# Kernel tuning notes

Measured on AMD Instinct MI355X. Metric: run time of the kernel, lower is better.

The kernel has to match this reference:

```python
import jax, jax.numpy as jnp
import numpy as np

N, E, C, ED = 50000, 800000, 128, 16
NEG_SLOPE = 0.2


def setup_inputs() -> dict:
    key = jax.random.key(0)
    ks = jax.random.split(key, 18)
    inp = {
        "h": jax.random.normal(ks[0], (N, C), jnp.float32),
        "edge_index": jax.random.randint(ks[1], (2, E), 0, N),
        "edge_attr": jax.random.normal(ks[2], (E, ED), jnp.float32),
        "reducible": jax.random.randint(ks[3], (N,), 0, 2) > 0,
    }
    names = ["W", "att_src", "att_dst", "W_edge", "att_edge", "W_res", "bias"]
    shapes = [(C, C), (C,), (C,), (ED, C), (C,), (C, C), (C,)]
    i = 4
    for pre in ["red_", "irr_"]:
        for n, sh in zip(names, shapes):
            inp[pre + n] = jax.random.normal(ks[i], sh, jnp.float32) * 0.05
            i += 1
    return inp


def _gat_conv(h, src, dst, edge_attr, W, att_src, att_dst, W_edge, att_edge, W_res, bias):
    """PyG GATConv (heads=1, residual=True, add_self_loops=True, fill_value='mean')."""
    n = h.shape[0]
    # self-loop edge_attr = mean of incoming edge_attr per node (0 if none)
    sum_attr = jax.ops.segment_sum(edge_attr, dst, num_segments=n)
    cnt = jax.ops.segment_sum(jnp.ones((edge_attr.shape[0],), edge_attr.dtype), dst, num_segments=n)
    mean_attr = sum_attr / jnp.maximum(cnt, 1.0)[:, None]
    loop = jnp.arange(n)
    s = jnp.concatenate([src, loop])   # [E+N]
    d = jnp.concatenate([dst, loop])   # [E+N]
    ea = jnp.concatenate([edge_attr, mean_attr], axis=0)  # [E+N, ED]
    x = h @ W                              # [N, C]
    a_src = x @ att_src                    # [N]
    a_dst = x @ att_dst                    # [N]
    a_edge = (ea @ W_edge) @ att_edge      # [E+N]
    alpha = jax.nn.leaky_relu(a_src[s] + a_dst[d] + a_edge, NEG_SLOPE)
    # per-destination softmax (every node has a self-loop -> denom > 0)
    m = jax.ops.segment_max(alpha, d, num_segments=n)
    ex = jnp.exp(alpha - m[d])
    denom = jax.ops.segment_sum(ex, d, num_segments=n)
    w = ex / denom[d]                      # [E+N]
    out = jax.ops.segment_sum(w[:, None] * x[s], d, num_segments=n)  # [N, C]
    return out + h @ W_res + bias


def reference(h, edge_index, edge_attr, reducible,
              red_W, red_att_src, red_att_dst, red_W_edge, red_att_edge, red_W_res, red_bias,
              irr_W, irr_att_src, irr_att_dst, irr_W_edge, irr_att_edge, irr_W_res, irr_bias):
    src, dst = edge_index[0], edge_index[1]
    out_r = _gat_conv(h, src, dst, edge_attr, red_W, red_att_src, red_att_dst,
                      red_W_edge, red_att_edge, red_W_res, red_bias)
    out_i = _gat_conv(h, src, dst, edge_attr, irr_W, irr_att_src, irr_att_dst,
                      irr_W_edge, irr_att_edge, irr_W_res, irr_bias)
    return jax.nn.relu(jnp.where(reducible[:, None], out_r, out_i))
```

## Files before the change

### kernel.cpp

```cpp
#include <hip/hip_runtime.h>
#include <hip/hip_bf16.h>

#define CDIM 128
#define EDIM 16
#define NEG_SLOPE 0.2f

typedef __attribute__((ext_vector_type(8))) short bf16x8;
typedef __attribute__((ext_vector_type(4))) float f32x4;
typedef unsigned int uint;
typedef unsigned short ushort;

__device__ __forceinline__ ushort f2bf(float f) {
    uint u = __float_as_uint(f);
    return (ushort)((u + 0x7fffu + ((u >> 16) & 1u)) >> 16);
}
__device__ __forceinline__ uint packbf(float lo, float hi) {
    return ((uint)f2bf(hi) << 16) | (uint)f2bf(lo);
}
__device__ __forceinline__ float bflo(uint w) { return __uint_as_float(w << 16); }
__device__ __forceinline__ float bfhi(uint w) { return __uint_as_float(w & 0xffff0000u); }

__device__ __forceinline__ bool redtest(const void* red, int i, int notInt, int notFloat) {
    if (!notInt)        return ((const int*)red)[i] != 0;
    else if (!notFloat) return ((const float*)red)[i] != 0.f;
    else                return ((const unsigned char*)red)[i] != 0;
}

__global__ void bcatwe_kernel(const float* __restrict__ Wr, const float* __restrict__ Wi,
                              const float* __restrict__ Wrr, const float* __restrict__ Wri,
                              ushort* __restrict__ BT,
                              const float* __restrict__ WeR, const float* __restrict__ aeR,
                              const float* __restrict__ WeI, const float* __restrict__ aeI,
                              float* __restrict__ we) {
    if (blockIdx.x < 256) {
        int idx = blockIdx.x * 256 + threadIdx.x;
        int c = idx >> 7, k = idx & 127;
        const float* srcm;
        if (c < 128)      srcm = Wr;
        else if (c < 256) srcm = Wi;
        else if (c < 384) srcm = Wrr;
        else              srcm = Wri;
        BT[idx] = f2bf(srcm[k * 128 + (c & 127)]);
    } else {
        int lane = threadIdx.x;
        if (lane < 16) {
            float s = 0.f;
            for (int c = 0; c < CDIM; ++c) s += WeR[lane * CDIM + c] * aeR[c];
            we[lane] = s;
        } else if (lane < 32) {
            int j = lane - 16;
            float s = 0.f;
            for (int c = 0; c < CDIM; ++c) s += WeI[j * CDIM + c] * aeI[c];
            we[16 + j] = s;
        }
    }
}

__global__ __launch_bounds__(256) void prep_kernel(const uint* __restrict__ red, int nwords,
                                                   int* __restrict__ flags,
                                                   const int* __restrict__ dst, int* __restrict__ cnt,
                                                   int* __restrict__ rank,
                                                   const float* __restrict__ ea, const float* __restrict__ we,
                                                   uint* __restrict__ escal4, int E) {
    int i = blockIdx.x * 256 + threadIdx.x;
    if (i < nwords) {
        uint w = red[i];
        bool isInt = (w <= 1u);
        bool isFloat = (w == 0u) || (w == 0x3f800000u);
        if (!isInt) atomicOr(&flags[0], 1);
        if (!isFloat) atomicOr(&flags[1], 1);
    }
    if (i < E) {
        rank[i] = atomicAdd(&cnt[dst[i]], 1);
        const float4* row = (const float4*)(ea + (size_t)i * EDIM);
        const float4* we4 = (const float4*)we;
        float er = 0.f, ei = 0.f;
#pragma unroll
        for (int q = 0; q < 4; ++q) {
            float4 v = row[q];
            float4 wr = we4[q], wi = we4[4 + q];
            er += v.x * wr.x + v.y * wr.y + v.z * wr.z + v.w * wr.w;
            ei += v.x * wi.x + v.y * wi.y + v.z * wi.z + v.w * wi.w;
        }
        escal4[i] = packbf(er, ei);
    }
}

__global__ __launch_bounds__(512) void gemm_fused(const float* __restrict__ h,
                                                  const ushort* __restrict__ BT,
                                                  ushort* __restrict__ C,
                                                  const float* __restrict__ attsr, const float* __restrict__ attdr,
                                                  const float* __restrict__ attsi, const float* __restrict__ attdi,
                                                  float* __restrict__ asr, float* __restrict__ adr,
                                                  float* __restrict__ asi, float* __restrict__ adi, int M) {
    __shared__ ushort Bs[512 * 128];
    __shared__ ushort As[64 * 128];
    __shared__ float dots[4][64];
    int t = threadIdx.x, lane = t & 63, wv = t >> 6;
    int rb = blockIdx.x * 64;
    int l15 = lane & 15, l4 = lane >> 4;

    if (t < 256) dots[t >> 6][t & 63] = 0.f;

#pragma unroll
    for (int p = 0; p < 16; ++p) {
        int g = wv * 16 + p;
        int col = g * 4 + l4;
        int chs = l15 ^ (col & 7);
        const ushort* gb = BT + col * 128 + chs * 8;
        __builtin_amdgcn_global_load_lds(
            (const __attribute__((address_space(1))) void*)gb,
            (__attribute__((address_space(3))) void*)((char*)Bs + g * 1024), 16, 0, 0);
    }

    {
        int row = t >> 3, cp = (t & 7) * 2;
        int gr = rb + row; if (gr > M - 1) gr = M - 1;
        const float4* hp = (const float4*)(h + (size_t)gr * 128 + cp * 8);
        float4 v0 = hp[0], v1 = hp[1], v2 = hp[2], v3 = hp[3];
        uint4 u0, u1;
        u0.x = packbf(v0.x, v0.y); u0.y = packbf(v0.z, v0.w);
        u0.z = packbf(v1.x, v1.y); u0.w = packbf(v1.z, v1.w);
        u1.x = packbf(v2.x, v2.y); u1.y = packbf(v2.z, v2.w);
        u1.z = packbf(v3.x, v3.y); u1.w = packbf(v3.z, v3.w);
        *(uint4*)((char*)As + row * 256 + ((cp)     ^ (row & 7)) * 16) = u0;
        *(uint4*)((char*)As + row * 256 + ((cp + 1) ^ (row & 7)) * 16) = u1;
    }
    __syncthreads();

    f32x4 acc[4][4];
#pragma unroll
    for (int i = 0; i < 4; ++i)
#pragma unroll
        for (int j = 0; j < 4; ++j) acc[i][j] = (f32x4){0.f, 0.f, 0.f, 0.f};

    const char* Ab = (const char*)As;
    const char* Bb = (const char*)Bs;
#pragma unroll
    for (int ks = 0; ks < 4; ++ks) {
        bf16x8 a[4], b[4];
#pragma unroll
        for (int f = 0; f < 4; ++f) {
            int row = f * 16 + l15;
            int ch = (ks * 4 + l4) ^ (row & 7);
            a[f] = *(const bf16x8*)(Ab + row * 256 + ch * 16);
            int col = wv * 64 + f * 16 + l15;
            int ch2 = (ks * 4 + l4) ^ (col & 7);
            b[f] = *(const bf16x8*)(Bb + col * 256 + ch2 * 16);
        }
#pragma unroll
        for (int i = 0; i < 4; ++i)
#pragma unroll
            for (int j = 0; j < 4; ++j)
                acc[i][j] = __builtin_amdgcn_mfma_f32_16x16x32_bf16(a[i], b[j], acc[i][j], 0, 0, 0);
    }

    if (wv < 4) {
        int var = wv >> 1;
        const float* attS = var ? attsi : attsr;
        const float* attD = var ? attdi : attdr;
        float aS[4], aD[4];
#pragma unroll
        for (int j = 0; j < 4; ++j) {
            int c = (wv & 1) * 64 + j * 16 + l15;
            aS[j] = attS[c]; aD[j] = attD[c];
        }
#pragma unroll
        for (int i = 0; i < 4; ++i)
#pragma unroll
            for (int rr = 0; rr < 4; ++rr) {
                float ps = 0.f, pd = 0.f;
#pragma unroll
                for (int j = 0; j < 4; ++j) {
                    float v = acc[i][j][rr];
                    ps += v * aS[j]; pd += v * aD[j];
                }
#pragma unroll
                for (int d = 1; d < 16; d <<= 1) {
                    ps += __shfl_xor(ps, d); pd += __shfl_xor(pd, d);
                }
                if (l15 == 0) {
                    int row = i * 16 + l4 * 4 + rr;
                    atomicAdd(&dots[var * 2 + 0][row], ps);
                    atomicAdd(&dots[var * 2 + 1][row], pd);
                }
            }
    }

#pragma unroll
    for (int i = 0; i < 4; ++i) {
#pragma unroll
        for (int j = 0; j < 4; ++j) {
            int col = wv * 64 + j * 16 + l15;
#pragma unroll
            for (int r = 0; r < 4; ++r) {
                int gr = rb + i * 16 + l4 * 4 + r;
                if (gr < M) C[(size_t)gr * 512 + col] = f2bf(acc[i][j][r]);
            }
        }
    }

    __syncthreads();
    if (t < 256) {
        int arr = t >> 6, row = t & 63;
        int gr = rb + row;
        if (gr < M) {
            float v = dots[arr][row];
            if (arr == 0)      asr[gr] = v;
            else if (arr == 1) adr[gr] = v;
            else if (arr == 2) asi[gr] = v;
            else               adi[gr] = v;
        }
    }
}

__global__ __launch_bounds__(256) void scanA_kernel(const int* __restrict__ cnt,
                                                    int* __restrict__ offv,
                                                    int* __restrict__ bsum, int n) {
    __shared__ int wsum[4];
    int t = threadIdx.x, lane = t & 63, wid = t >> 6;
    int i0 = blockIdx.x * 1024 + t * 4;
    int v[4];
#pragma unroll
    for (int j = 0; j < 4; ++j) { int i = i0 + j; v[j] = (i < n) ? cnt[i] : 0; }
    int s = v[0] + v[1] + v[2] + v[3];
    int incl = s;
#pragma unroll
    for (int d = 1; d < 64; d <<= 1) { int u = __shfl_up(incl, d); if (lane >= d) incl += u; }
    if (lane == 63) wsum[wid] = incl;
    __syncthreads();
    int wpre = 0;
    for (int w = 0; w < wid; ++w) wpre += wsum[w];
    int run = wpre + incl - s;
#pragma unroll
    for (int j = 0; j < 4; ++j) {
        int i = i0 + j;
        if (i < n) offv[i] = run;
        run += v[j];
    }
    if (t == 255) bsum[blockIdx.x] = wpre + incl;
}

__global__ void scanB_kernel(int* __restrict__ bsum, int* __restrict__ offv, int nb, int n) {
    int lane = threadIdx.x;
    int carry = 0;
    for (int base = 0; base < nb; base += 64) {
        int i = base + lane;
        int v = (i < nb) ? bsum[i] : 0;
        int incl = v;
#pragma unroll
        for (int d = 1; d < 64; d <<= 1) { int u = __shfl_up(incl, d); if (lane >= d) incl += u; }
        if (i < nb) bsum[i] = carry + incl - v;
        carry += __shfl(incl, 63);
    }
    if (lane == 0) offv[n] = carry;
}

__global__ __launch_bounds__(256) void scanC_kernel(int* __restrict__ offv,
                                                    const int* __restrict__ bsum, int n) {
    int add = bsum[blockIdx.x];
    int i0 = blockIdx.x * 1024 + threadIdx.x * 4;
#pragma unroll
    for (int j = 0; j < 4; ++j) {
        int i = i0 + j;
        if (i < n) offv[i] += add;
    }
}

__global__ __launch_bounds__(256) void scatter_kernel(
    const int* __restrict__ src, const int* __restrict__ dst,
    const int* __restrict__ rank, const uint* __restrict__ escal4,
    const void* __restrict__ red, const int* __restrict__ flags,
    const int* __restrict__ offv, uint* __restrict__ csr, int E) {
    int e = blockIdx.x * 256 + threadIdx.x;
    if (e >= E) return;
    int s = src[e], d = dst[e];
    uint ee = escal4[e];
    int notInt = flags[0], notFloat = flags[1];
    bool rr = redtest(red, d, notInt, notFloat);
    uint evb = rr ? (ee & 0xffffu) : (ee >> 16);
    csr[offv[d] + rank[e]] = (uint)s | (evb << 16);
}

__global__ __launch_bounds__(256) void node_kernel(
    const ushort* __restrict__ xcat,
    const float* __restrict__ adst_r, const float* __restrict__ adst_i,
    const float* __restrict__ asrc_r, const float* __restrict__ asrc_i,
    const void* __restrict__ red, const int* __restrict__ flags,
    const int* __restrict__ offv, const uint* __restrict__ csr,
    const float* __restrict__ bias_r, const float* __restrict__ bias_i,
    float* __restrict__ out, int n) {
    __shared__ uint2 buf[4][64];
    int wv = threadIdx.x >> 6, lane = threadIdx.x & 63;
    int node = blockIdx.x * 4 + wv;
    if (node >= n) return;

    int notInt = flags[0], notFloat = flags[1];
    bool r = redtest(red, node, notInt, notFloat);

    const float* asrc = r ? asrc_r : asrc_i;
    float adst = (r ? adst_r : adst_i)[node];
    uint vsel = r ? 0u : 256u;
    int b0 = offv[node], b1 = offv[node + 1];
    int k = b1 - b0;
    const char* xb = (const char*)xcat;
    uint lane4 = lane * 4;

    float m = -1e30f, denom = 0.f;
    float acc0a = 0.f, acc1a = 0.f, acc0b = 0.f, acc1b = 0.f;
    float sumE = 0.f;

    for (int base = b0; base < b1; base += 64) {
        int j = base + lane;
        float al = -1e30f; uint soff = 0;
        if (j < b1) {
            uint rec = csr[j];
            uint s = rec & 0xffffu;
            float ev = bfhi(rec);
            sumE += ev;
            soff = s * 1024u + vsel;
            float a = asrc[s] + ev + adst;
            al = (a >= 0.f) ? a : NEG_SLOPE * a;
        }
        float cm = al;
#pragma unroll
        for (int d = 32; d; d >>= 1) cm = fmaxf(cm, __shfl_xor(cm, d));
        float mn = fmaxf(m, cm);
        float sc = __expf(m - mn);
        denom *= sc; acc0a *= sc; acc1a *= sc; acc0b *= sc; acc1b *= sc;
        m = mn;
        float ex = (j < b1) ? __expf(al - mn) : 0.f;
        buf[wv][lane] = make_uint2(__float_as_uint(ex), soff);
        __builtin_amdgcn_wave_barrier();
        int cc = min(64, b1 - base);
        int ccp = (cc + 7) & ~7;
        for (int tq = 0; tq < ccp; tq += 8) {
            uint2 u[8];
#pragma unroll
            for (int q = 0; q < 8; ++q) u[q] = buf[wv][tq + q];
            uint v[8];
#pragma unroll
            for (int q = 0; q < 8; ++q) v[q] = *(const uint*)(xb + u[q].y + lane4);
#pragma unroll
            for (int q = 0; q < 4; ++q) {
                float w = __uint_as_float(u[q].x);
                acc0a += w * bflo(v[q]); acc1a += w * bfhi(v[q]);
            }
#pragma unroll
            for (int q = 4; q < 8; ++q) {
                float w = __uint_as_float(u[q].x);
                acc0b += w * bflo(v[q]); acc1b += w * bfhi(v[q]);
            }
        }
        float exs = ex;
#pragma unroll
        for (int d = 32; d; d >>= 1) exs += __shfl_xor(exs, d);
        denom += exs;
        __builtin_amdgcn_wave_barrier();
    }
    float acc0 = acc0a + acc0b, acc1 = acc1a + acc1b;

#pragma unroll
    for (int d = 32; d; d >>= 1) sumE += __shfl_xor(sumE, d);
    float eself = sumE / fmaxf((float)k, 1.f);
    float a = asrc[node] + adst + eself;
    float aself = (a >= 0.f) ? a : NEG_SLOPE * a;
    float mn = fmaxf(m, aself);
    float sc = __expf(m - mn);
    float exl = __expf(aself - mn);
    denom = denom * sc + exl;
    uint voff = (uint)node * 1024u + vsel;
    uint vsw = *(const uint*)(xb + voff + lane4);
    acc0 = acc0 * sc + exl * bflo(vsw);
    acc1 = acc1 * sc + exl * bfhi(vsw);

    float inv = 1.f / denom;
    uint roff = (uint)node * 1024u + (r ? 512u : 768u);
    uint bw = *(const uint*)(xb + roff + lane4);
    float2 bi2 = ((const float2*)(r ? bias_r : bias_i))[lane];
    float o0 = acc0 * inv + bflo(bw) + bi2.x;
    float o1 = acc1 * inv + bfhi(bw) + bi2.y;
    ((float2*)out)[(size_t)node * 64 + lane] = make_float2(fmaxf(o0, 0.f), fmaxf(o1, 0.f));
}

extern "C" void kernel_launch(void* const* d_in, const int* in_sizes, int n_in,
                              void* d_out, int out_size, void* d_ws, size_t ws_size,
                              hipStream_t stream) {
    const float* h          = (const float*)d_in[0];
    const int*   edge_index = (const int*)d_in[1];
    const float* edge_attr  = (const float*)d_in[2];
    const void*  reducible  = d_in[3];
    const float* red_W      = (const float*)d_in[4];
    const float* red_att_src= (const float*)d_in[5];
    const float* red_att_dst= (const float*)d_in[6];
    const float* red_W_edge = (const float*)d_in[7];
    const float* red_att_edge=(const float*)d_in[8];
    const float* red_W_res  = (const float*)d_in[9];
    const float* red_bias   = (const float*)d_in[10];
    const float* irr_W      = (const float*)d_in[11];
    const float* irr_att_src= (const float*)d_in[12];
    const float* irr_att_dst= (const float*)d_in[13];
    const float* irr_W_edge = (const float*)d_in[14];
    const float* irr_att_edge=(const float*)d_in[15];
    const float* irr_W_res  = (const float*)d_in[16];
    const float* irr_bias   = (const float*)d_in[17];

    const int N = in_sizes[0] / CDIM;
    const int E = in_sizes[1] / 2;
    const int* src = edge_index;
    const int* dst = edge_index + E;
    const int nb = (N + 1023) / 1024;

    float* out = (float*)d_out;

    size_t cur = 0;
    auto alloc = [&](size_t bytes) { size_t p = cur; cur = (cur + bytes + 255) & ~(size_t)255; return p; };
    char* ws = (char*)d_ws;
    size_t o_xcat  = alloc((size_t)N * 512 * 2);
    size_t o_bcat  = alloc(512 * 128 * 2);
    size_t o_we    = alloc(256);
    size_t o_asr   = alloc((size_t)N * 4);
    size_t o_adr   = alloc((size_t)N * 4);
    size_t o_asi   = alloc((size_t)N * 4);
    size_t o_adi   = alloc((size_t)N * 4);
    size_t o_flags = alloc(256);
    size_t o_cnt   = alloc((size_t)N * 4);
    size_t o_off   = alloc((size_t)(N + 1) * 4);
    size_t o_bsum  = alloc((size_t)(nb + 1) * 4);
    size_t o_rank  = alloc((size_t)E * 4);
    size_t o_escal = alloc((size_t)E * 4);
    size_t o_csr   = alloc((size_t)E * 4);
    if (cur > ws_size) return;

    ushort* xcat = (ushort*)(ws + o_xcat);
    ushort* bcat = (ushort*)(ws + o_bcat);
    float* we    = (float*)(ws + o_we);
    float* asr   = (float*)(ws + o_asr);
    float* adr   = (float*)(ws + o_adr);
    float* asi   = (float*)(ws + o_asi);
    float* adi   = (float*)(ws + o_adi);
    int*   flags = (int*)(ws + o_flags);
    int*   cnt   = (int*)(ws + o_cnt);
    int*   offv  = (int*)(ws + o_off);
    int*   bsum  = (int*)(ws + o_bsum);
    int*   rank  = (int*)(ws + o_rank);
    uint*  escal4= (uint*)(ws + o_escal);
    uint*  csr   = (uint*)(ws + o_csr);

    hipMemsetAsync(flags, 0, 8, stream);
    hipMemsetAsync(cnt, 0, (size_t)N * 4, stream);

    bcatwe_kernel<<<257, 256, 0, stream>>>(red_W, irr_W, red_W_res, irr_W_res, bcat,
                                           red_W_edge, red_att_edge, irr_W_edge, irr_att_edge, we);

    int nwords = N / 4;
    prep_kernel<<<(E + 255) / 256, 256, 0, stream>>>((const uint*)reducible, nwords, flags,
                                                     dst, cnt, rank, edge_attr, we, escal4, E);

    gemm_fused<<<(N + 63) / 64, 512, 0, stream>>>(h, bcat, xcat,
                                                  red_att_src, red_att_dst,
                                                  irr_att_src, irr_att_dst,
                                                  asr, adr, asi, adi, N);

    scanA_kernel<<<nb, 256, 0, stream>>>(cnt, offv, bsum, N);
    scanB_kernel<<<1, 64, 0, stream>>>(bsum, offv, nb, N);
    scanC_kernel<<<nb, 256, 0, stream>>>(offv, bsum, N);

    scatter_kernel<<<(E + 255) / 256, 256, 0, stream>>>(src, dst, rank, escal4,
                                                        reducible, flags, offv, csr, E);

    node_kernel<<<(N + 3) / 4, 256, 0, stream>>>(xcat, adr, adi, asr, asi,
                                                 reducible, flags, offv, csr,
                                                 red_bias, irr_bias, out, N);
}
```

Before: 156.6 us.

## Pre-convert h to bf16 in prep kernel and retile GEMM into 128x128 blocks

Moves the fp32-to-bf16 conversion of h into the edge prep kernel, which writes a new bf16 copy in workspace. The fused GEMM is replaced by a 2D-grid kernel with 128x128 output tiles and 256 threads, loading both A and B straight to LDS with async global_load_lds. Attention dot products are now computed only by column blocks 0 and 1. The aim is to cut the per-block B reload (the whole 512x128 weight per 64 rows before) and raise occupancy, at the cost of an extra bf16 round trip of h through memory and four blocks per row tile each re-reading A.

```diff
diff --git a/kernel.cpp b/kernel.cpp
--- a/kernel.cpp
+++ b/kernel.cpp
@@ -61,7 +61,9 @@
                                                    const int* __restrict__ dst, int* __restrict__ cnt,
                                                    int* __restrict__ rank,
                                                    const float* __restrict__ ea, const float* __restrict__ we,
-                                                   uint* __restrict__ escal4, int E) {
+                                                   uint* __restrict__ escal4,
+                                                   const float* __restrict__ h, ushort* __restrict__ hbf,
+                                                   int E, int n4) {
     int i = blockIdx.x * 256 + threadIdx.x;
     if (i < nwords) {
         uint w = red[i];
@@ -84,50 +86,53 @@
         }
         escal4[i] = packbf(er, ei);
     }
-}
-
-__global__ __launch_bounds__(512) void gemm_fused(const float* __restrict__ h,
-                                                  const ushort* __restrict__ BT,
-                                                  ushort* __restrict__ C,
-                                                  const float* __restrict__ attsr, const float* __restrict__ attdr,
-                                                  const float* __restrict__ attsi, const float* __restrict__ attdi,
-                                                  float* __restrict__ asr, float* __restrict__ adr,
-                                                  float* __restrict__ asi, float* __restrict__ adi, int M) {
-    __shared__ ushort Bs[512 * 128];
-    __shared__ ushort As[64 * 128];
-    __shared__ float dots[4][64];
-    int t = threadIdx.x, lane = t & 63, wv = t >> 6;
-    int rb = blockIdx.x * 64;
-    int l15 = lane & 15, l4 = lane >> 4;
-
-    if (t < 256) dots[t >> 6][t & 63] = 0.f;
-
-#pragma unroll
-    for (int p = 0; p < 16; ++p) {
-        int g = wv * 16 + p;
-        int col = g * 4 + l4;
-        int chs = l15 ^ (col & 7);
-        const ushort* gb = BT + col * 128 + chs * 8;
+    if (i < n4) {
+        float4 v = ((const float4*)h)[i];
+        ushort4 o;
+        o.x = f2bf(v.x); o.y = f2bf(v.y); o.z = f2bf(v.z); o.w = f2bf(v.w);
+        ((ushort4*)hbf)[i] = o;
+    }
+}
+
+__global__ __launch_bounds__(256) void gemm_dots(const ushort* __restrict__ A,
+                                                 const ushort* __restrict__ BT,
+                                                 ushort* __restrict__ C,
+                                                 const float* __restrict__ attsr, const float* __restrict__ attdr,
+                                                 const float* __restrict__ attsi, const float* __restrict__ attdi,
+                                                 float* __restrict__ asr, float* __restrict__ adr,
+                                                 float* __restrict__ asi, float* __restrict__ adi, int M) {
+    __shared__ ushort As[128 * 128];
+    __shared__ ushort Bs[128 * 128];
+    __shared__ float dots[2][128];
+    int t = threadIdx.x;
+    int lane = t & 63, wv = t >> 6;
+    int rb = blockIdx.x * 128, cb = blockIdx.y * 128;
+    int by = blockIdx.y;
+
+    if (t < 128) { dots[0][t] = 0.f; dots[1][t] = 0.f; }
+
+    int rsub = wv * 4 + (lane >> 4);
+    int c0 = lane & 15;
+#pragma unroll
+    for (int p = 0; p < 8; ++p) {
+        int row = p * 16 + rsub;
+        int chunk = c0 ^ (row & 7);
+        int gra = rb + row; if (gra > M - 1) gra = M - 1;
+        const ushort* ga = A + (size_t)gra * 128 + chunk * 8;
+        __builtin_amdgcn_global_load_lds(
+            (const __attribute__((address_space(1))) void*)ga,
+            (__attribute__((address_space(3))) void*)((char*)As + p * 4096 + wv * 1024),
+            16, 0, 0);
+        const ushort* gb = BT + (size_t)(cb + row) * 128 + chunk * 8;
         __builtin_amdgcn_global_load_lds(
             (const __attribute__((address_space(1))) void*)gb,
-            (__attribute__((address_space(3))) void*)((char*)Bs + g * 1024), 16, 0, 0);
-    }
-
-    {
-        int row = t >> 3, cp = (t & 7) * 2;
-        int gr = rb + row; if (gr > M - 1) gr = M - 1;
-        const float4* hp = (const float4*)(h + (size_t)gr * 128 + cp * 8);
-        float4 v0 = hp[0], v1 = hp[1], v2 = hp[2], v3 = hp[3];
-        uint4 u0, u1;
-        u0.x = packbf(v0.x, v0.y); u0.y = packbf(v0.z, v0.w);
-        u0.z = packbf(v1.x, v1.y); u0.w = packbf(v1.z, v1.w);
-        u1.x = packbf(v2.x, v2.y); u1.y = packbf(v2.z, v2.w);
-        u1.z = packbf(v3.x, v3.y); u1.w = packbf(v3.z, v3.w);
-        *(uint4*)((char*)As + row * 256 + ((cp)     ^ (row & 7)) * 16) = u0;
-        *(uint4*)((char*)As + row * 256 + ((cp + 1) ^ (row & 7)) * 16) = u1;
+            (__attribute__((address_space(3))) void*)((char*)Bs + p * 4096 + wv * 1024),
+            16, 0, 0);
     }
     __syncthreads();
 
+    int wr = wv >> 1, wc = wv & 1;
+    int l15 = lane & 15, l4 = lane >> 4;
     f32x4 acc[4][4];
 #pragma unroll
     for (int i = 0; i < 4; ++i)
@@ -141,10 +146,10 @@
         bf16x8 a[4], b[4];
 #pragma unroll
         for (int f = 0; f < 4; ++f) {
-            int row = f * 16 + l15;
+            int row = wr * 64 + f * 16 + l15;
             int ch = (ks * 4 + l4) ^ (row & 7);
             a[f] = *(const bf16x8*)(Ab + row * 256 + ch * 16);
-            int col = wv * 64 + f * 16 + l15;
+            int col = wc * 64 + f * 16 + l15;
             int ch2 = (ks * 4 + l4) ^ (col & 7);
             b[f] = *(const bf16x8*)(Bb + col * 256 + ch2 * 16);
         }
@@ -155,14 +160,13 @@
                 acc[i][j] = __builtin_amdgcn_mfma_f32_16x16x32_bf16(a[i], b[j], acc[i][j], 0, 0, 0);
     }
 
-    if (wv < 4) {
-        int var = wv >> 1;
-        const float* attS = var ? attsi : attsr;
-        const float* attD = var ? attdi : attdr;
+    if (by < 2) {
+        const float* attS = by ? attsi : attsr;
+        const float* attD = by ? attdi : attdr;
         float aS[4], aD[4];
 #pragma unroll
         for (int j = 0; j < 4; ++j) {
-            int c = (wv & 1) * 64 + j * 16 + l15;
+            int c = wc * 64 + j * 16 + l15;
             aS[j] = attS[c]; aD[j] = attD[c];
         }
 #pragma unroll
@@ -180,36 +184,35 @@
                     ps += __shfl_xor(ps, d); pd += __shfl_xor(pd, d);
                 }
                 if (l15 == 0) {
-                    int row = i * 16 + l4 * 4 + rr;
-                    atomicAdd(&dots[var * 2 + 0][row], ps);
-                    atomicAdd(&dots[var * 2 + 1][row], pd);
+                    int row = wr * 64 + i * 16 + l4 * 4 + rr;
+                    atomicAdd(&dots[0][row], ps);
+                    atomicAdd(&dots[1][row], pd);
                 }
             }
     }
 
 #pragma unroll
     for (int i = 0; i < 4; ++i) {
+        int rl = wr * 64 + i * 16 + l4 * 4;
 #pragma unroll
         for (int j = 0; j < 4; ++j) {
-            int col = wv * 64 + j * 16 + l15;
+            int col = cb + wc * 64 + j * 16 + l15;
 #pragma unroll
             for (int r = 0; r < 4; ++r) {
-                int gr = rb + i * 16 + l4 * 4 + r;
+                int gr = rb + rl + r;
                 if (gr < M) C[(size_t)gr * 512 + col] = f2bf(acc[i][j][r]);
             }
         }
     }
 
-    __syncthreads();
-    if (t < 256) {
-        int arr = t >> 6, row = t & 63;
-        int gr = rb + row;
-        if (gr < M) {
-            float v = dots[arr][row];
-            if (arr == 0)      asr[gr] = v;
-            else if (arr == 1) adr[gr] = v;
-            else if (arr == 2) asi[gr] = v;
-            else               adi[gr] = v;
+    if (by < 2) {
+        __syncthreads();
+        if (t < 128) {
+            int gr = rb + t;
+            if (gr < M) {
+                if (by == 0) { asr[gr] = dots[0][t]; adr[gr] = dots[1][t]; }
+                else         { asi[gr] = dots[0][t]; adi[gr] = dots[1][t]; }
+            }
         }
     }
 }
@@ -410,6 +413,7 @@
     const int* src = edge_index;
     const int* dst = edge_index + E;
     const int nb = (N + 1023) / 1024;
+    const int n4 = N * 128 / 4;
 
     float* out = (float*)d_out;
 
@@ -417,6 +421,7 @@
     auto alloc = [&](size_t bytes) { size_t p = cur; cur = (cur + bytes + 255) & ~(size_t)255; return p; };
     char* ws = (char*)d_ws;
     size_t o_xcat  = alloc((size_t)N * 512 * 2);
+    size_t o_hbf   = alloc((size_t)N * 128 * 2);
     size_t o_bcat  = alloc(512 * 128 * 2);
     size_t o_we    = alloc(256);
     size_t o_asr   = alloc((size_t)N * 4);
@@ -433,6 +438,7 @@
     if (cur > ws_size) return;
 
     ushort* xcat = (ushort*)(ws + o_xcat);
+    ushort* hbf  = (ushort*)(ws + o_hbf);
     ushort* bcat = (ushort*)(ws + o_bcat);
     float* we    = (float*)(ws + o_we);
     float* asr   = (float*)(ws + o_asr);
@@ -454,13 +460,16 @@
                                            red_W_edge, red_att_edge, irr_W_edge, irr_att_edge, we);
 
     int nwords = N / 4;
-    prep_kernel<<<(E + 255) / 256, 256, 0, stream>>>((const uint*)reducible, nwords, flags,
-                                                     dst, cnt, rank, edge_attr, we, escal4, E);
-
-    gemm_fused<<<(N + 63) / 64, 512, 0, stream>>>(h, bcat, xcat,
-                                                  red_att_src, red_att_dst,
-                                                  irr_att_src, irr_att_dst,
-                                                  asr, adr, asi, adi, N);
+    int pgrid = (max(E, n4) + 255) / 256;
+    prep_kernel<<<pgrid, 256, 0, stream>>>((const uint*)reducible, nwords, flags,
+                                           dst, cnt, rank, edge_attr, we, escal4,
+                                           h, hbf, E, n4);
+
+    dim3 ggrid((N + 127) / 128, 4);
+    gemm_dots<<<ggrid, 256, 0, stream>>>(hbf, bcat, xcat,
+                                         red_att_src, red_att_dst,
+                                         irr_att_src, irr_att_dst,
+                                         asr, adr, asi, adi, N);
 
     scanA_kernel<<<nb, 256, 0, stream>>>(cnt, offv, bsum, N);
     scanB_kernel<<<1, 64, 0, stream>>>(bsum, offv, nb, N);
```

Measured after the change: 148.8 us. 1.05x faster.
